# Performance work log

Measured on AMD Instinct MI355X. Metric: run time of the kernel, lower is better.

## Reference

```python
import jax, jax.numpy as jnp
import numpy as np

B, T, N, F_IN = 8, 288, 2000, 1
E, ID, H, K = 128, 16, 128, 20
FL = T // 2 + 1  # rfft length = in_len//2 + 1
EPS_NORM = 1e-12
EPS_LN = 1e-8


def setup_inputs() -> dict:
    key = jax.random.key(0)
    k0, k1, k2, k3, k4 = jax.random.split(key, 5)
    return {
        "x": jax.random.normal(k0, (B, T, N, F_IN), jnp.float32),
        "Ex": jax.random.normal(k1, (FL, E), jnp.float32),
        "nodes": jax.random.normal(k2, (N, ID), jnp.float32),
        "Wd": jax.random.normal(k3, (N, E + ID, H), jnp.float32),
        "Wxabs": jax.random.normal(k4, (H, H), jnp.float32),
    }


def reference(x, Ex, nodes, Wd, Wxabs):
    # [B,T,N,F] -> take feature 0 -> [B,N,T]
    xt = jnp.transpose(x[:, :, :, 0], (0, 2, 1))
    xf = jnp.abs(jnp.fft.rfft(xt, axis=-1))  # [B,N,FL]
    # F.normalize p=2 over dim=1 (nodes), then dim=2 (freq): x / max(||x||, eps)
    xf = xf / jnp.clip(jnp.sqrt(jnp.sum(xf * xf, axis=1, keepdims=True)), EPS_NORM)
    xf = xf / jnp.clip(jnp.sqrt(jnp.sum(xf * xf, axis=2, keepdims=True)), EPS_NORM)
    xe = jnp.matmul(xf, Ex)  # [B,N,E]
    # cat(): append static node identity embedding per batch element
    xk = jnp.concatenate(
        [xe, jnp.broadcast_to(nodes, (xe.shape[0], N, ID))], axis=-1
    )  # [B,N,E+ID]
    # per-node weight bmm: [N,B,E+ID] @ [N,E+ID,H] -> [B,N,H]
    x1 = jax.nn.relu(jnp.einsum('bnd,ndh->bnh', xk, Wd))
    # LayerNorm over last two dims [N,H], eps=1e-8, no affine
    mu = jnp.mean(x1, axis=(1, 2), keepdims=True)
    var = jnp.mean((x1 - mu) ** 2, axis=(1, 2), keepdims=True)
    x2 = (x1 - mu) / jnp.sqrt(var + EPS_LN)
    # dropout is identity at inference
    adp = jnp.einsum('bnh,hk->bnk', x2, Wxabs)  # convt
    adj = jnp.einsum('bnh,bmh->bnm', adp, x1)  # [B,N,N]
    adp = jax.nn.relu(adj)
    # dy_mask_graph: per-row topk over dim=2 (torch dim=1 of the [N,N] slice),
    # binary mask via scatter of ones, then elementwise mask
    _, idx = jax.lax.top_k(adp, K)  # [B,N,K]
    bi = jnp.arange(adp.shape[0])[:, None, None]
    ni = jnp.arange(N)[None, :, None]
    mask = jnp.zeros_like(adp).at[bi, ni, idx].set(1.0)
    adj_masked = adp * mask
    return jax.nn.softmax(adj_masked, axis=2)
```

## Files before the change

kernel.cpp:

```cpp
#include <hip/hip_runtime.h>
#include <math.h>

#define BB 8
#define TT 288
#define NN 2000
#define FLEN 145
#define EE 128
#define IDD 16
#define HH 128
#define DKK 144
#define KTOP 20

typedef _Float16 half8 __attribute__((ext_vector_type(8)));
typedef float f32x4 __attribute__((ext_vector_type(4)));
typedef unsigned short ushort_t;

#define OFF_TW  ((size_t)0)
#define SZ_TW   ((size_t)TT*FLEN*2)
#define OFF_XF  (OFF_TW + SZ_TW)
#define SZ_XF   ((size_t)BB*FLEN*NN)
#define OFF_ICN (OFF_XF + SZ_XF)
#define OFF_IRN (OFF_ICN + (size_t)BB*FLEN)
#define OFF_XE  (OFF_IRN + (size_t)BB*NN)
#define SZ_BNH  ((size_t)BB*NN*HH)
#define OFF_X1  (OFF_XE + SZ_BNH)
#define OFF_ADP (OFF_X1 + SZ_BNH)
#define OFF_CSW (OFF_ADP + SZ_BNH)
#define OFF_LNS (OFF_CSW + HH)
#define OFF_LNF (OFF_LNS + 16)


__device__ __forceinline__ float wredSum(float v) {
#pragma unroll
  for (int o = 32; o > 0; o >>= 1) v += __shfl_down(v, o, 64);
  return v;
}
__device__ __forceinline__ float wredMax(float v) {
#pragma unroll
  for (int o = 32; o > 0; o >>= 1) v = fmaxf(v, __shfl_down(v, o, 64));
  return v;
}
__device__ __forceinline__ float wredSumAll(float v) {
#pragma unroll
  for (int o = 32; o > 0; o >>= 1) v += __shfl_xor(v, o, 64);
  return v;
}
__device__ __forceinline__ float wredMaxAll(float v) {
#pragma unroll
  for (int o = 32; o > 0; o >>= 1) v = fmaxf(v, __shfl_xor(v, o, 64));
  return v;
}

__device__ __forceinline__ void split16(float v, ushort_t& hi, ushort_t& lo) {
  _Float16 h = (_Float16)v;
  _Float16 l = (_Float16)(v - (float)h);
  union { _Float16 f; ushort_t u; } a, b;
  a.f = h; b.f = l;
  hi = a.u; lo = b.u;
}

__global__ void k_init(const float* __restrict__ Wx, float* __restrict__ csw,
                       float* __restrict__ lns) {
  int k = threadIdx.x;
  float s = 0.f;
  for (int h = 0; h < HH; ++h) s += Wx[h * HH + k];
  csw[k] = s;
  if (k < 16) lns[k] = 0.f;
}

__global__ void k_tw(float* __restrict__ tw) {
  int id = blockIdx.x * 256 + threadIdx.x;
  if (id >= TT * FLEN) return;
  int t = id / FLEN, f = id % FLEN;
  int r = (t * f) % TT;
  double th = -2.0 * 3.14159265358979323846 * (double)r / (double)TT;
  tw[2 * id]     = (float)cos(th);
  tw[2 * id + 1] = (float)sin(th);
}

__global__ void k_dft(const float* __restrict__ x, const float* __restrict__ tw,
                      float* __restrict__ xf) {
  __shared__ __align__(16) float Xs[16][128];
  __shared__ __align__(16) float TWs[16][32][2];
  const int b = blockIdx.z;
  const int f0 = blockIdx.y * 32;
  const int n0 = blockIdx.x * 128;
  const int tid = threadIdx.x;
  const int tn = tid & 31;
  const int tf = tid >> 5;
  float ar[4][4] = {}, ai[4][4] = {};
  for (int t0 = 0; t0 < TT; t0 += 16) {
    __syncthreads();
    for (int l = tid; l < 512; l += 256) {
      int row = l >> 5, q = l & 31;
      int n = n0 + q * 4;
      const float* src = x + ((size_t)b * TT + (t0 + row)) * NN + n;
      float4 v = make_float4(0, 0, 0, 0);
      if (n + 3 < NN) v = *(const float4*)src;
      else {
        if (n + 0 < NN) v.x = src[0];
        if (n + 1 < NN) v.y = src[1];
        if (n + 2 < NN) v.z = src[2];
        if (n + 3 < NN) v.w = src[3];
      }
      *(float4*)&Xs[row][q * 4] = v;
    }
    for (int l = tid; l < 512; l += 256) {
      int row = l >> 5, ff = l & 31;
      int f = f0 + ff;
      float2 cs = make_float2(0, 0);
      if (f < FLEN) cs = *(const float2*)&tw[((size_t)(t0 + row) * FLEN + f) * 2];
      *(float2*)&TWs[row][ff][0] = cs;
    }
    __syncthreads();
#pragma unroll 4
    for (int t = 0; t < 16; ++t) {
      float4 xv = *(float4*)&Xs[t][tn * 4];
      float xx[4] = {xv.x, xv.y, xv.z, xv.w};
      float4 p0 = *(float4*)&TWs[t][tf * 4][0];
      float4 p1 = *(float4*)&TWs[t][tf * 4 + 2][0];
      float c[4] = {p0.x, p0.z, p1.x, p1.z};
      float s[4] = {p0.y, p0.w, p1.y, p1.w};
#pragma unroll
      for (int i = 0; i < 4; ++i)
#pragma unroll
        for (int j = 0; j < 4; ++j) {
          ar[i][j] = fmaf(xx[j], c[i], ar[i][j]);
          ai[i][j] = fmaf(xx[j], s[i], ai[i][j]);
        }
    }
  }
#pragma unroll
  for (int i = 0; i < 4; ++i) {
    int f = f0 + tf * 4 + i;
    if (f >= FLEN) continue;
    float* dst = &xf[((size_t)b * FLEN + f) * NN];
    float o[4];
#pragma unroll
    for (int j = 0; j < 4; ++j)
      o[j] = sqrtf(ar[i][j] * ar[i][j] + ai[i][j] * ai[i][j]);
    int n = n0 + tn * 4;
    if (n + 3 < NN) *(float4*)&dst[n] = make_float4(o[0], o[1], o[2], o[3]);
    else {
#pragma unroll
      for (int j = 0; j < 4; ++j) if (n + j < NN) dst[n + j] = o[j];
    }
  }
}

__global__ void k_colnorm(const float* __restrict__ xf, float* __restrict__ icn) {
  __shared__ float sc[4];
  int bf = blockIdx.x;
  const float* rowp = xf + (size_t)bf * NN;
  float s = 0.f;
  for (int i = threadIdx.x; i < NN; i += 256) { float v = rowp[i]; s = fmaf(v, v, s); }
  s = wredSum(s);
  int lane = threadIdx.x & 63, w = threadIdx.x >> 6;
  if (lane == 0) sc[w] = s;
  __syncthreads();
  if (threadIdx.x == 0)
    icn[bf] = 1.f / fmaxf(sqrtf(sc[0] + sc[1] + sc[2] + sc[3]), 1e-12f);
}

__global__ void k_rownorm(const float* __restrict__ xf, const float* __restrict__ icn,
                          float* __restrict__ irn) {
  int b = blockIdx.y;
  int n = blockIdx.x * 256 + threadIdx.x;
  if (n >= NN) return;
  float s = 0.f;
  for (int f = 0; f < FLEN; ++f) {
    float v = xf[((size_t)b * FLEN + f) * NN + n] * icn[b * FLEN + f];
    s = fmaf(v, v, s);
  }
  irn[b * NN + n] = 1.f / fmaxf(sqrtf(s), 1e-12f);
}

__global__ void k_xe(const float* __restrict__ xf, const float* __restrict__ icn,
                     const float* __restrict__ irn, const float* __restrict__ Ex,
                     float* __restrict__ xe) {
  __shared__ __align__(16) float As[16][64];
  __shared__ __align__(16) float Bs[16][128];
  const int b = blockIdx.y;
  const int n0 = blockIdx.x * 64;
  const int tid = threadIdx.x;
  const int tn = tid >> 4, te = tid & 15;
  float acc[4][8] = {};
  for (int f0 = 0; f0 < 160; f0 += 16) {
    __syncthreads();
    {
      int kt = tid >> 4, q = tid & 15;
      int f = f0 + kt;
      int n = n0 + q * 4;
      float4 v = make_float4(0, 0, 0, 0);
      if (f < FLEN) {
        float ic = icn[b * FLEN + f];
        const float* src = &xf[((size_t)b * FLEN + f) * NN + n];
        if (n + 3 < NN) v = *(const float4*)src;
        else {
          if (n + 0 < NN) v.x = src[0];
          if (n + 1 < NN) v.y = src[1];
          if (n + 2 < NN) v.z = src[2];
          if (n + 3 < NN) v.w = src[3];
        }
        v.x *= ic; v.y *= ic; v.z *= ic; v.w *= ic;
      }
      *(float4*)&As[kt][q * 4] = v;
    }
    for (int l = tid; l < 512; l += 256) {
      int kt = l >> 5, q = l & 31;
      int f = f0 + kt;
      float4 v = make_float4(0, 0, 0, 0);
      if (f < FLEN) v = *(const float4*)&Ex[(size_t)f * EE + q * 4];
      *(float4*)&Bs[kt][q * 4] = v;
    }
    __syncthreads();
#pragma unroll
    for (int k = 0; k < 16; ++k) {
      float4 a  = *(float4*)&As[k][tn * 4];
      float4 b0 = *(float4*)&Bs[k][te * 4];
      float4 b1 = *(float4*)&Bs[k][64 + te * 4];
      float av[4] = {a.x, a.y, a.z, a.w};
      float bv[8] = {b0.x, b0.y, b0.z, b0.w, b1.x, b1.y, b1.z, b1.w};
#pragma unroll
      for (int i = 0; i < 4; ++i)
#pragma unroll
        for (int j = 0; j < 8; ++j)
          acc[i][j] = fmaf(av[i], bv[j], acc[i][j]);
    }
  }
#pragma unroll
  for (int i = 0; i < 4; ++i) {
    int n = n0 + tn * 4 + i;
    if (n >= NN) continue;
    float sc = irn[b * NN + n];
    float* dst = &xe[((size_t)b * NN + n) * EE];
    *(float4*)&dst[te * 4] =
        make_float4(acc[i][0] * sc, acc[i][1] * sc, acc[i][2] * sc, acc[i][3] * sc);
    *(float4*)&dst[64 + te * 4] =
        make_float4(acc[i][4] * sc, acc[i][5] * sc, acc[i][6] * sc, acc[i][7] * sc);
  }
}

__global__ void k_x1(const float* xe, const float* __restrict__ nodes,
                     const float* __restrict__ Wd, float* __restrict__ x1,
                     ushort_t* x1hl) {
  __shared__ __align__(16) float xk[8][DKK];
  __shared__ float red[4][32][33];
  const int n = blockIdx.x;
  const int tid = threadIdx.x;
  {
    int b = tid >> 5, q = tid & 31;
    *(float4*)&xk[b][q * 4] = *(const float4*)&xe[((size_t)b * NN + n) * EE + q * 4];
  }
  if (tid < 128) {
    int b = tid >> 4, i = tid & 15;
    xk[b][EE + i] = nodes[(size_t)n * IDD + i];
  }
  __syncthreads();
  const int h4 = tid & 31;
  const int dg = tid >> 5;
  float acc[8][4] = {};
  for (int d = dg; d < DKK; d += 8) {
    float4 wv = *(const float4*)&Wd[((size_t)n * DKK + d) * HH + h4 * 4];
#pragma unroll
    for (int b = 0; b < 8; ++b) {
      float xv = xk[b][d];
      acc[b][0] = fmaf(xv, wv.x, acc[b][0]);
      acc[b][1] = fmaf(xv, wv.y, acc[b][1]);
      acc[b][2] = fmaf(xv, wv.z, acc[b][2]);
      acc[b][3] = fmaf(xv, wv.w, acc[b][3]);
    }
  }
#pragma unroll
  for (int b = 0; b < 8; ++b)
#pragma unroll
    for (int j = 0; j < 4; ++j)
      acc[b][j] += __shfl_xor(acc[b][j], 32, 64);
  const int wv_ = tid >> 6, lane = tid & 63;
  if (lane < 32) {
#pragma unroll
    for (int b = 0; b < 8; ++b)
#pragma unroll
      for (int j = 0; j < 4; ++j)
        red[wv_][lane][b * 4 + j] = acc[b][j];
  }
  __syncthreads();
  const size_t tbase = (size_t)(n >> 4) * 4096 + (size_t)(n & 15) * 8;
#pragma unroll
  for (int o = 0; o < 4; ++o) {
    int idx = tid + o * 256;
    int b = idx >> 7, h = idx & 127;
    float s = red[0][h >> 2][b * 4 + (h & 3)] + red[1][h >> 2][b * 4 + (h & 3)] +
              red[2][h >> 2][b * 4 + (h & 3)] + red[3][h >> 2][b * 4 + (h & 3)];
    s = fmaxf(s, 0.f);
    x1[((size_t)b * NN + n) * HH + h] = s;
    ushort_t hi, lo;
    split16(s, hi, lo);
    size_t slot = (size_t)b * (125 * 4096) + tbase +
                  (size_t)((h >> 5) * 512 + ((h >> 3) & 3) * 128 + (h & 7));
    x1hl[slot] = hi;
    x1hl[slot + 2048] = lo;
  }
}

__global__ void k_ln_stats(const float* __restrict__ x1, float* __restrict__ lns) {
  __shared__ float sc[4], sc2[4];
  int b = blockIdx.y, chunk = blockIdx.x;
  const float* base = x1 + (size_t)b * NN * HH + (size_t)chunk * 8000;
  float s = 0.f, s2 = 0.f;
  for (int i = threadIdx.x; i < 8000; i += 256) {
    float v = base[i];
    s += v; s2 = fmaf(v, v, s2);
  }
  s = wredSum(s); s2 = wredSum(s2);
  int lane = threadIdx.x & 63, w = threadIdx.x >> 6;
  if (lane == 0) { sc[w] = s; sc2[w] = s2; }
  __syncthreads();
  if (threadIdx.x == 0) {
    atomicAdd(&lns[b], sc[0] + sc[1] + sc[2] + sc[3]);
    atomicAdd(&lns[8 + b], sc2[0] + sc2[1] + sc2[2] + sc2[3]);
  }
}

__global__ void k_ln_final(const float* __restrict__ lns, float* __restrict__ lnf) {
  int b = threadIdx.x;
  if (b < 8) {
    float cnt = (float)(NN * HH);
    float mu = lns[b] / cnt;
    float var = fmaxf(lns[8 + b] / cnt - mu * mu, 0.f);
    lnf[b] = mu;
    lnf[8 + b] = 1.f / sqrtf(var + 1e-8f);
  }
}

__global__ void k_adp(const float* __restrict__ x1, const float* __restrict__ Wx,
                      const float* __restrict__ csw, const float* __restrict__ lnf,
                      ushort_t* __restrict__ adphl) {
  __shared__ __align__(16) float As[16][64];
  __shared__ __align__(16) float Bs[16][128];
  const int r0 = blockIdx.x * 64;
  const int tid = threadIdx.x;
  const int tn = tid >> 4, te = tid & 15;
  float acc[4][8] = {};
  for (int k0 = 0; k0 < HH; k0 += 16) {
    __syncthreads();
    {
      int rr = tid >> 2, kq = tid & 3;
      float4 v = *(const float4*)&x1[(size_t)(r0 + rr) * HH + k0 + kq * 4];
      As[kq * 4 + 0][rr] = v.x;
      As[kq * 4 + 1][rr] = v.y;
      As[kq * 4 + 2][rr] = v.z;
      As[kq * 4 + 3][rr] = v.w;
    }
    for (int l = tid; l < 512; l += 256) {
      int kt = l >> 5, q = l & 31;
      *(float4*)&Bs[kt][q * 4] = *(const float4*)&Wx[(size_t)(k0 + kt) * HH + q * 4];
    }
    __syncthreads();
#pragma unroll
    for (int k = 0; k < 16; ++k) {
      float4 a  = *(float4*)&As[k][tn * 4];
      float4 b0 = *(float4*)&Bs[k][te * 4];
      float4 b1 = *(float4*)&Bs[k][64 + te * 4];
      float av[4] = {a.x, a.y, a.z, a.w};
      float bv[8] = {b0.x, b0.y, b0.z, b0.w, b1.x, b1.y, b1.z, b1.w};
#pragma unroll
      for (int i = 0; i < 4; ++i)
#pragma unroll
        for (int j = 0; j < 8; ++j)
          acc[i][j] = fmaf(av[i], bv[j], acc[i][j]);
    }
  }
  float4 c0 = *(const float4*)&csw[te * 4];
  float4 c1 = *(const float4*)&csw[64 + te * 4];
  float cw[8] = {c0.x, c0.y, c0.z, c0.w, c1.x, c1.y, c1.z, c1.w};
  const int c0k = te * 4, c1k = 64 + te * 4;
  const size_t o0r = (size_t)((c0k >> 5) * 512 + ((c0k >> 3) & 3) * 128 + (c0k & 7));
  const size_t o1r = (size_t)((c1k >> 5) * 512 + ((c1k >> 3) & 3) * 128 + (c1k & 7));
#pragma unroll
  for (int i = 0; i < 4; ++i) {
    int r = r0 + tn * 4 + i;
    int b = r / NN, n = r % NN;
    float mu = lnf[b], isd = lnf[8 + b];
    ushort_t hi[8], lo[8];
#pragma unroll
    for (int j = 0; j < 8; ++j) {
      float o = (acc[i][j] - mu * cw[j]) * isd;
      split16(o, hi[j], lo[j]);
    }
    size_t slot = (size_t)b * (125 * 4096) + (size_t)(n >> 4) * 4096 +
                  (size_t)(n & 15) * 8;
    ushort4 u;
    u.x = hi[0]; u.y = hi[1]; u.z = hi[2]; u.w = hi[3];
    *(ushort4*)&adphl[slot + o0r] = u;
    u.x = hi[4]; u.y = hi[5]; u.z = hi[6]; u.w = hi[7];
    *(ushort4*)&adphl[slot + o1r] = u;
    u.x = lo[0]; u.y = lo[1]; u.z = lo[2]; u.w = lo[3];
    *(ushort4*)&adphl[slot + 2048 + o0r] = u;
    u.x = lo[4]; u.y = lo[5]; u.z = lo[6]; u.w = lo[7];
    *(ushort4*)&adphl[slot + 2048 + o1r] = u;
  }
}

__global__ __launch_bounds__(256, 2) void k_adjT(
    const ushort_t* __restrict__ adphl, const ushort_t* __restrict__ x1hl,
    float* __restrict__ out) {
  const int b = blockIdx.z;
  const int tA = blockIdx.y;
  const int n0 = tA * 16;
  const int tid = threadIdx.x;
  const int w = tid >> 6;
  const int lane = tid & 63;
  const int quad = lane >> 4, r16 = lane & 15;
  const int lq = quad * 128 + r16 * 8;

  half8 Ah[4], Al[4];
  {
    const ushort_t* abase = adphl + ((size_t)(b * 125 + tA)) * 4096 + lq;
#pragma unroll
    for (int ks = 0; ks < 4; ++ks) {
      Ah[ks] = *(const half8*)(abase + ks * 512);
      Al[ks] = *(const half8*)(abase + 2048 + ks * 512);
    }
  }
  const int mbase = blockIdx.x * 512 + w * 128;
  const ushort_t* Bb = x1hl + (size_t)b * (125 * 4096) + lq;
  float* obase = out + ((size_t)(b * NN + n0 + quad * 4)) * NN;

  half8 Bh0[4], Bl0[4], Bh1[4], Bl1[4];

#define LOADB(I, BH, BL)                                                      \
  {                                                                           \
    int tB_ = (mbase + (I) * 16) >> 4;                                        \
    if (tB_ > 124) tB_ = 124;         \
    const ushort_t* bb_ = Bb + (size_t)tB_ * 4096;                            \
    BH[0] = *(const half8*)(bb_);        BL[0] = *(const half8*)(bb_ + 2048); \
    BH[1] = *(const half8*)(bb_ + 512);  BL[1] = *(const half8*)(bb_ + 2560); \
    BH[2] = *(const half8*)(bb_ + 1024); BL[2] = *(const half8*)(bb_ + 3072); \
    BH[3] = *(const half8*)(bb_ + 1536); BL[3] = *(const half8*)(bb_ + 3584); \
  }

#define STEP(I, BH, BL, BH2, BL2)                                             \
  {                                                                           \
    if ((I) < 7) LOADB((I) + 1, BH2, BL2);                                    \
    __builtin_amdgcn_sched_barrier(0);      \
    f32x4 acc = (f32x4){0.f, 0.f, 0.f, 0.f};                                  \
    _Pragma("unroll")                                                         \
    for (int ks = 0; ks < 4; ++ks) {                                          \
      acc = __builtin_amdgcn_mfma_f32_16x16x32_f16(Ah[ks], BH[ks], acc, 0, 0, 0); \
      acc = __builtin_amdgcn_mfma_f32_16x16x32_f16(Ah[ks], BL[ks], acc, 0, 0, 0); \
      acc = __builtin_amdgcn_mfma_f32_16x16x32_f16(Al[ks], BH[ks], acc, 0, 0, 0); \
    }                                                                         \
    int mt_ = mbase + (I) * 16 + r16;                                         \
    if (mt_ < NN) {                                                           \
      _Pragma("unroll")                                                       \
      for (int reg = 0; reg < 4; ++reg)                                       \
        obase[(size_t)reg * NN + mt_] = fmaxf(acc[reg], 0.f);                 \
    }                                                                         \
  }

  LOADB(0, Bh0, Bl0);
  STEP(0, Bh0, Bl0, Bh1, Bl1);
  STEP(1, Bh1, Bl1, Bh0, Bl0);
  STEP(2, Bh0, Bl0, Bh1, Bl1);
  STEP(3, Bh1, Bl1, Bh0, Bl0);
  STEP(4, Bh0, Bl0, Bh1, Bl1);
  STEP(5, Bh1, Bl1, Bh0, Bl0);
  STEP(6, Bh0, Bl0, Bh1, Bl1);
  STEP(7, Bh1, Bl1, Bh0, Bl0);
#undef STEP
#undef LOADB
}

__global__ __launch_bounds__(256, 4) void k_topsm(float* out) {
  __shared__ float scrV[4][64];
  __shared__ int scrI[4][64];
  const int tid = threadIdx.x;
  const int w = tid >> 6, lane = tid & 63;
  const int r = blockIdx.x * 4 + w;
  float* g = out + (size_t)r * NN;

  f32x4 V[8];
#pragma unroll
  for (int j = 0; j < 8; ++j) {
    int m0 = j * 256 + lane * 4;
    if (m0 < NN) V[j] = *(const f32x4*)&g[m0];
    else V[j] = (f32x4){-1.f, -1.f, -1.f, -1.f};
  }

  float mx = -1.f, cp = 0.f;
#pragma unroll
  for (int j = 0; j < 8; ++j)
#pragma unroll
    for (int e = 0; e < 4; ++e) {
      mx = fmaxf(mx, V[j][e]);
      cp += (V[j][e] > 0.f) ? 1.f : 0.f;
    }
  const float m = wredMaxAll(mx);
  const float cpos = wredSumAll(cp);
  const float em = expf(-m);

  if (cpos <= 20.5f) {
    float s = 0.f;
#pragma unroll
    for (int j = 0; j < 8; ++j)
#pragma unroll
      for (int e = 0; e < 4; ++e)
        if (V[j][e] > 0.f) s += expf(V[j][e] - m);
    s = wredSumAll(s);
    const float invD = 1.f / (s + (2000.f - cpos) * em);
    const float defv = em * invD;
#pragma unroll
    for (int j = 0; j < 8; ++j) {
      int m0 = j * 256 + lane * 4;
      if (m0 >= NN) continue;
      float4 o;
      o.x = (V[j][0] > 0.f) ? expf(V[j][0] - m) * invD : defv;
      o.y = (V[j][1] > 0.f) ? expf(V[j][1] - m) * invD : defv;
      o.z = (V[j][2] > 0.f) ? expf(V[j][2] - m) * invD : defv;
      o.w = (V[j][3] > 0.f) ? expf(V[j][3] - m) * invD : defv;
      *(float4*)&g[m0] = o;
    }
  } else {
    float tval = 0.f, cf = cpos;
    if (cpos > 64.5f) {
      float tlo = 0.f, thi = m;
      bool found = false;
      for (int it = 0; it < 64 && !found; ++it) {
        float mid = (it < 12)
            ? 0.5f * (tlo + thi)
            : __uint_as_float((__float_as_uint(tlo) + __float_as_uint(thi)) >> 1);
        float c = 0.f;
#pragma unroll
        for (int j = 0; j < 8; ++j)
#pragma unroll
          for (int e = 0; e < 4; ++e)
            c += (V[j][e] > mid) ? 1.f : 0.f;
        c = wredSumAll(c);
        if (c > 64.5f) tlo = mid;
        else if (c < 19.5f) thi = mid;
        else { tval = mid; cf = c; found = true; }
      }
      if (!found) { tval = tlo; cf = 64.f; }
    }
    int cI = (int)(cf + 0.5f);
    if (cI > 64) cI = 64;

    float* sv = scrV[w];
    int* si = scrI[w];
    int base = 0;
#pragma unroll
    for (int j = 0; j < 8; ++j)
#pragma unroll
      for (int e = 0; e < 4; ++e) {
        bool p = V[j][e] > tval;
        unsigned long long msk = __ballot(p);
        if (p) {
          int pos = base + (int)__popcll(msk & ((1ull << lane) - 1ull));
          if (pos < 64) { sv[pos] = V[j][e]; si[pos] = j * 256 + lane * 4 + e; }
        }
        base += (int)__popcll(msk);
      }
    asm volatile("s_waitcnt lgkmcnt(0)" ::: "memory");

    float cv = (lane < cI) ? sv[lane] : -1.f;
    int ci = (lane < cI) ? si[lane] : 0x7fffffff;
#pragma unroll
    for (int k = 2; k <= 64; k <<= 1)
#pragma unroll
      for (int j = k >> 1; j > 0; j >>= 1) {
        float ov = __shfl_xor(cv, j, 64);
        int oi = __shfl_xor(ci, j, 64);
        bool otherBetter = (ov > cv) || (ov == cv && oi < ci);
        bool iAmLow = (lane & j) == 0;
        bool desc = (lane & k) == 0;
        bool take = (desc == iAmLow) ? otherBetter : !otherBetter;
        if (take) { cv = ov; ci = oi; }
      }
    const float t20 = __shfl(cv, 19, 64);
    float e20 = (lane < 20) ? expf(cv - m) : 0.f;
    const float s20 = wredSumAll(e20);
    const float invD = 1.f / (s20 + (2000.f - 20.f) * em);
    const float defv = em * invD;
#pragma unroll
    for (int j = 0; j < 8; ++j) {
      int m0 = j * 256 + lane * 4;
      if (m0 >= NN) continue;
      float4 o;
      o.x = (V[j][0] >= t20) ? expf(V[j][0] - m) * invD : defv;
      o.y = (V[j][1] >= t20) ? expf(V[j][1] - m) * invD : defv;
      o.z = (V[j][2] >= t20) ? expf(V[j][2] - m) * invD : defv;
      o.w = (V[j][3] >= t20) ? expf(V[j][3] - m) * invD : defv;
      *(float4*)&g[m0] = o;
    }
  }
}

extern "C" void kernel_launch(void* const* d_in, const int* in_sizes, int n_in,
                              void* d_out, int out_size, void* d_ws, size_t ws_size,
                              hipStream_t stream) {
  const float* x     = (const float*)d_in[0];
  const float* Ex    = (const float*)d_in[1];
  const float* nodes = (const float*)d_in[2];
  const float* Wd    = (const float*)d_in[3];
  const float* Wx    = (const float*)d_in[4];
  float* out = (float*)d_out;
  float* w = (float*)d_ws;
  float* tw  = w + OFF_TW;
  float* xf  = w + OFF_XF;
  float* icn = w + OFF_ICN;
  float* irn = w + OFF_IRN;
  float* xe  = w + OFF_XE;
  float* x1  = w + OFF_X1;
  float* csw = w + OFF_CSW;
  float* lns = w + OFF_LNS;
  float* lnf = w + OFF_LNF;
  ushort_t* adphl = (ushort_t*)(w + OFF_ADP);
  ushort_t* x1hl  = (ushort_t*)(w + OFF_XE);

  k_init<<<1, 128, 0, stream>>>(Wx, csw, lns);
  k_tw<<<(TT * FLEN + 255) / 256, 256, 0, stream>>>(tw);
  k_dft<<<dim3(16, 5, BB), 256, 0, stream>>>(x, tw, xf);
  k_colnorm<<<BB * FLEN, 256, 0, stream>>>(xf, icn);
  k_rownorm<<<dim3(8, BB), 256, 0, stream>>>(xf, icn, irn);
  k_xe<<<dim3(32, BB), 256, 0, stream>>>(xf, icn, irn, Ex, xe);
  k_x1<<<NN, 256, 0, stream>>>(xe, nodes, Wd, x1, x1hl);
  k_ln_stats<<<dim3(32, BB), 256, 0, stream>>>(x1, lns);
  k_ln_final<<<1, 64, 0, stream>>>(lns, lnf);
  k_adp<<<250, 256, 0, stream>>>(x1, Wx, csw, lnf, adphl);
  k_adjT<<<dim3(4, 125, BB), 256, 0, stream>>>(adphl, x1hl, out);
  k_topsm<<<(BB * NN) / 4, 256, 0, stream>>>(out);
}
```

Before: 490.7 us.

## Fuse adjacency GEMM with top-k softmax and merge tiny init kernels

The adjacency MFMA kernel now computes a full 16-row by 2000-column strip per 512-thread block and keeps it in registers. It then does the per-row max, count, bisection threshold search, candidate collection and softmax in place, so the intermediate [B,N,N] matrix is no longer written and re-read by a separate top-k pass. The small init and LN-finalize kernels are folded into the twiddle and adp kernels to cut launches. In exchange, register pressure goes up, the grid has only 1000 blocks, and the bisection loop needs block-wide syncs.

```diff
diff --git a/kernel.cpp b/kernel.cpp
--- a/kernel.cpp
+++ b/kernel.cpp
@@ -35,19 +35,9 @@
   for (int o = 32; o > 0; o >>= 1) v += __shfl_down(v, o, 64);
   return v;
 }
-__device__ __forceinline__ float wredMax(float v) {
-#pragma unroll
-  for (int o = 32; o > 0; o >>= 1) v = fmaxf(v, __shfl_down(v, o, 64));
-  return v;
-}
 __device__ __forceinline__ float wredSumAll(float v) {
 #pragma unroll
   for (int o = 32; o > 0; o >>= 1) v += __shfl_xor(v, o, 64);
-  return v;
-}
-__device__ __forceinline__ float wredMaxAll(float v) {
-#pragma unroll
-  for (int o = 32; o > 0; o >>= 1) v = fmaxf(v, __shfl_xor(v, o, 64));
   return v;
 }
 
@@ -59,16 +49,15 @@
   hi = a.u; lo = b.u;
 }
 
-__global__ void k_init(const float* __restrict__ Wx, float* __restrict__ csw,
-                       float* __restrict__ lns) {
-  int k = threadIdx.x;
-  float s = 0.f;
-  for (int h = 0; h < HH; ++h) s += Wx[h * HH + k];
-  csw[k] = s;
-  if (k < 16) lns[k] = 0.f;
-}
-
-__global__ void k_tw(float* __restrict__ tw) {
+__global__ void k_tw(const float* __restrict__ Wx, float* __restrict__ tw,
+                     float* __restrict__ csw, float* __restrict__ lns) {
+  if (blockIdx.x == 0 && threadIdx.x < 128) {
+    int k = threadIdx.x;
+    float s = 0.f;
+    for (int h = 0; h < HH; ++h) s += Wx[h * HH + k];
+    csw[k] = s;
+    if (k < 16) lns[k] = 0.f;
+  }
   int id = blockIdx.x * 256 + threadIdx.x;
   if (id >= TT * FLEN) return;
   int t = id / FLEN, f = id % FLEN;
@@ -322,19 +311,8 @@
   }
 }
 
-__global__ void k_ln_final(const float* __restrict__ lns, float* __restrict__ lnf) {
-  int b = threadIdx.x;
-  if (b < 8) {
-    float cnt = (float)(NN * HH);
-    float mu = lns[b] / cnt;
-    float var = fmaxf(lns[8 + b] / cnt - mu * mu, 0.f);
-    lnf[b] = mu;
-    lnf[8 + b] = 1.f / sqrtf(var + 1e-8f);
-  }
-}
-
 __global__ void k_adp(const float* __restrict__ x1, const float* __restrict__ Wx,
-                      const float* __restrict__ csw, const float* __restrict__ lnf,
+                      const float* __restrict__ csw, const float* __restrict__ lns,
                       ushort_t* __restrict__ adphl) {
   __shared__ __align__(16) float As[16][64];
   __shared__ __align__(16) float Bs[16][128];
@@ -381,7 +359,10 @@
   for (int i = 0; i < 4; ++i) {
     int r = r0 + tn * 4 + i;
     int b = r / NN, n = r % NN;
-    float mu = lnf[b], isd = lnf[8 + b];
+    float cnt = (float)(NN * HH);
+    float mu = lns[b] / cnt;
+    float var = fmaxf(lns[8 + b] / cnt - mu * mu, 0.f);
+    float isd = 1.f / sqrtf(var + 1e-8f);
     ushort_t hi[8], lo[8];
 #pragma unroll
     for (int j = 0; j < 8; ++j) {
@@ -402,11 +383,18 @@
   }
 }
 
-__global__ __launch_bounds__(256, 2) void k_adjT(
+__global__ __launch_bounds__(512, 2) void k_adjsm(
     const ushort_t* __restrict__ adphl, const ushort_t* __restrict__ x1hl,
     float* __restrict__ out) {
-  const int b = blockIdx.z;
-  const int tA = blockIdx.y;
+  __shared__ float wmax[8][16], wcnt0[8][16], wcntB[8][16], wexp[8][16];
+  __shared__ int doneP[16];
+  __shared__ int candCnt[16];
+  __shared__ float candV[16][64];
+  __shared__ int candI[16][64];
+  __shared__ float pthr[16], pm[16], pinv[16], pdef[16];
+
+  const int b = blockIdx.y;
+  const int tA = blockIdx.x;
   const int n0 = tA * 16;
   const int tid = threadIdx.x;
   const int w = tid >> 6;
@@ -423,17 +411,15 @@
       Al[ks] = *(const half8*)(abase + 2048 + ks * 512);
     }
   }
-  const int mbase = blockIdx.x * 512 + w * 128;
   const ushort_t* Bb = x1hl + (size_t)b * (125 * 4096) + lq;
-  float* obase = out + ((size_t)(b * NN + n0 + quad * 4)) * NN;
-
+  f32x4 V[16];
   half8 Bh0[4], Bl0[4], Bh1[4], Bl1[4];
 
 #define LOADB(I, BH, BL)                                                      \
   {                                                                           \
-    int tB_ = (mbase + (I) * 16) >> 4;                                        \
-    if (tB_ > 124) tB_ = 124;         \
-    const ushort_t* bb_ = Bb + (size_t)tB_ * 4096;                            \
+    int tl_ = w + 8 * (I);                                                    \
+    if (tl_ > 124) tl_ = 124;                                                 \
+    const ushort_t* bb_ = Bb + (size_t)tl_ * 4096;                            \
     BH[0] = *(const half8*)(bb_);        BL[0] = *(const half8*)(bb_ + 2048); \
     BH[1] = *(const half8*)(bb_ + 512);  BL[1] = *(const half8*)(bb_ + 2560); \
     BH[2] = *(const half8*)(bb_ + 1024); BL[2] = *(const half8*)(bb_ + 3072); \
@@ -442,8 +428,8 @@
 
 #define STEP(I, BH, BL, BH2, BL2)                                             \
   {                                                                           \
-    if ((I) < 7) LOADB((I) + 1, BH2, BL2);                                    \
-    __builtin_amdgcn_sched_barrier(0);      \
+    if ((I) < 15) LOADB((I) + 1, BH2, BL2);                                   \
+    __builtin_amdgcn_sched_barrier(0);                                        \
     f32x4 acc = (f32x4){0.f, 0.f, 0.f, 0.f};                                  \
     _Pragma("unroll")                                                         \
     for (int ks = 0; ks < 4; ++ks) {                                          \
@@ -451,147 +437,225 @@
       acc = __builtin_amdgcn_mfma_f32_16x16x32_f16(Ah[ks], BL[ks], acc, 0, 0, 0); \
       acc = __builtin_amdgcn_mfma_f32_16x16x32_f16(Al[ks], BH[ks], acc, 0, 0, 0); \
     }                                                                         \
-    int mt_ = mbase + (I) * 16 + r16;                                         \
-    if (mt_ < NN) {                                                           \
-      _Pragma("unroll")                                                       \
-      for (int reg = 0; reg < 4; ++reg)                                       \
-        obase[(size_t)reg * NN + mt_] = fmaxf(acc[reg], 0.f);                 \
-    }                                                                         \
+    bool vld_ = (w + 8 * (I)) <= 124;                                         \
+    _Pragma("unroll")                                                         \
+    for (int reg = 0; reg < 4; ++reg)                                         \
+      V[(I)][reg] = vld_ ? fmaxf(acc[reg], 0.f) : -1.f;                       \
   }
 
   LOADB(0, Bh0, Bl0);
-  STEP(0, Bh0, Bl0, Bh1, Bl1);
-  STEP(1, Bh1, Bl1, Bh0, Bl0);
-  STEP(2, Bh0, Bl0, Bh1, Bl1);
-  STEP(3, Bh1, Bl1, Bh0, Bl0);
-  STEP(4, Bh0, Bl0, Bh1, Bl1);
-  STEP(5, Bh1, Bl1, Bh0, Bl0);
-  STEP(6, Bh0, Bl0, Bh1, Bl1);
-  STEP(7, Bh1, Bl1, Bh0, Bl0);
+  STEP(0,  Bh0, Bl0, Bh1, Bl1);
+  STEP(1,  Bh1, Bl1, Bh0, Bl0);
+  STEP(2,  Bh0, Bl0, Bh1, Bl1);
+  STEP(3,  Bh1, Bl1, Bh0, Bl0);
+  STEP(4,  Bh0, Bl0, Bh1, Bl1);
+  STEP(5,  Bh1, Bl1, Bh0, Bl0);
+  STEP(6,  Bh0, Bl0, Bh1, Bl1);
+  STEP(7,  Bh1, Bl1, Bh0, Bl0);
+  STEP(8,  Bh0, Bl0, Bh1, Bl1);
+  STEP(9,  Bh1, Bl1, Bh0, Bl0);
+  STEP(10, Bh0, Bl0, Bh1, Bl1);
+  STEP(11, Bh1, Bl1, Bh0, Bl0);
+  STEP(12, Bh0, Bl0, Bh1, Bl1);
+  STEP(13, Bh1, Bl1, Bh0, Bl0);
+  STEP(14, Bh0, Bl0, Bh1, Bl1);
+  STEP(15, Bh1, Bl1, Bh0, Bl0);
 #undef STEP
 #undef LOADB
-}
-
-__global__ __launch_bounds__(256, 4) void k_topsm(float* out) {
-  __shared__ float scrV[4][64];
-  __shared__ int scrI[4][64];
-  const int tid = threadIdx.x;
-  const int w = tid >> 6, lane = tid & 63;
-  const int r = blockIdx.x * 4 + w;
-  float* g = out + (size_t)r * NN;
-
-  f32x4 V[8];
-#pragma unroll
-  for (int j = 0; j < 8; ++j) {
-    int m0 = j * 256 + lane * 4;
-    if (m0 < NN) V[j] = *(const f32x4*)&g[m0];
-    else V[j] = (f32x4){-1.f, -1.f, -1.f, -1.f};
-  }
-
-  float mx = -1.f, cp = 0.f;
-#pragma unroll
-  for (int j = 0; j < 8; ++j)
-#pragma unroll
-    for (int e = 0; e < 4; ++e) {
-      mx = fmaxf(mx, V[j][e]);
-      cp += (V[j][e] > 0.f) ? 1.f : 0.f;
-    }
-  const float m = wredMaxAll(mx);
-  const float cpos = wredSumAll(cp);
-  const float em = expf(-m);
-
-  if (cpos <= 20.5f) {
-    float s = 0.f;
-#pragma unroll
-    for (int j = 0; j < 8; ++j)
-#pragma unroll
-      for (int e = 0; e < 4; ++e)
-        if (V[j][e] > 0.f) s += expf(V[j][e] - m);
-    s = wredSumAll(s);
-    const float invD = 1.f / (s + (2000.f - cpos) * em);
-    const float defv = em * invD;
-#pragma unroll
-    for (int j = 0; j < 8; ++j) {
-      int m0 = j * 256 + lane * 4;
-      if (m0 >= NN) continue;
-      float4 o;
-      o.x = (V[j][0] > 0.f) ? expf(V[j][0] - m) * invD : defv;
-      o.y = (V[j][1] > 0.f) ? expf(V[j][1] - m) * invD : defv;
-      o.z = (V[j][2] > 0.f) ? expf(V[j][2] - m) * invD : defv;
-      o.w = (V[j][3] > 0.f) ? expf(V[j][3] - m) * invD : defv;
-      *(float4*)&g[m0] = o;
-    }
-  } else {
-    float tval = 0.f, cf = cpos;
-    if (cpos > 64.5f) {
-      float tlo = 0.f, thi = m;
-      bool found = false;
-      for (int it = 0; it < 64 && !found; ++it) {
-        float mid = (it < 12)
-            ? 0.5f * (tlo + thi)
-            : __uint_as_float((__float_as_uint(tlo) + __float_as_uint(thi)) >> 1);
-        float c = 0.f;
-#pragma unroll
-        for (int j = 0; j < 8; ++j)
-#pragma unroll
-          for (int e = 0; e < 4; ++e)
-            c += (V[j][e] > mid) ? 1.f : 0.f;
-        c = wredSumAll(c);
-        if (c > 64.5f) tlo = mid;
-        else if (c < 19.5f) thi = mid;
-        else { tval = mid; cf = c; found = true; }
+
+  float mx4[4] = {-1.f, -1.f, -1.f, -1.f}, cp4[4] = {0.f, 0.f, 0.f, 0.f};
+#pragma unroll
+  for (int i = 0; i < 16; ++i)
+#pragma unroll
+    for (int reg = 0; reg < 4; ++reg) {
+      mx4[reg] = fmaxf(mx4[reg], V[i][reg]);
+      cp4[reg] += (V[i][reg] > 0.f) ? 1.f : 0.f;
+    }
+#pragma unroll
+  for (int o = 8; o > 0; o >>= 1)
+#pragma unroll
+    for (int reg = 0; reg < 4; ++reg) {
+      mx4[reg] = fmaxf(mx4[reg], __shfl_xor(mx4[reg], o, 64));
+      cp4[reg] += __shfl_xor(cp4[reg], o, 64);
+    }
+  if (r16 == 0) {
+#pragma unroll
+    for (int reg = 0; reg < 4; ++reg) {
+      wmax[w][quad * 4 + reg] = mx4[reg];
+      wcnt0[w][quad * 4 + reg] = cp4[reg];
+    }
+  }
+  __syncthreads();
+  float m4[4], c4[4];
+#pragma unroll
+  for (int reg = 0; reg < 4; ++reg) {
+    int row = quad * 4 + reg;
+    float m = wmax[0][row], c = wcnt0[0][row];
+    for (int ww = 1; ww < 8; ++ww) { m = fmaxf(m, wmax[ww][row]); c += wcnt0[ww][row]; }
+    m4[reg] = m; c4[reg] = c;
+  }
+
+  float se4[4] = {0.f, 0.f, 0.f, 0.f};
+#pragma unroll
+  for (int reg = 0; reg < 4; ++reg) {
+    if (c4[reg] <= 20.5f) {
+#pragma unroll
+      for (int i = 0; i < 16; ++i) {
+        float v = V[i][reg];
+        if (v > 0.f) se4[reg] += expf(v - m4[reg]);
       }
-      if (!found) { tval = tlo; cf = 64.f; }
-    }
-    int cI = (int)(cf + 0.5f);
-    if (cI > 64) cI = 64;
-
-    float* sv = scrV[w];
-    int* si = scrI[w];
-    int base = 0;
-#pragma unroll
-    for (int j = 0; j < 8; ++j)
-#pragma unroll
-      for (int e = 0; e < 4; ++e) {
-        bool p = V[j][e] > tval;
-        unsigned long long msk = __ballot(p);
-        if (p) {
-          int pos = base + (int)__popcll(msk & ((1ull << lane) - 1ull));
-          if (pos < 64) { sv[pos] = V[j][e]; si[pos] = j * 256 + lane * 4 + e; }
+    }
+  }
+#pragma unroll
+  for (int o = 8; o > 0; o >>= 1)
+#pragma unroll
+    for (int reg = 0; reg < 4; ++reg) se4[reg] += __shfl_xor(se4[reg], o, 64);
+  if (r16 == 0)
+#pragma unroll
+    for (int reg = 0; reg < 4; ++reg) wexp[w][quad * 4 + reg] = se4[reg];
+
+  float tlo4[4], thi4[4], tval4[4];
+  int done4[4];
+#pragma unroll
+  for (int reg = 0; reg < 4; ++reg) {
+    tval4[reg] = 0.f;
+    tlo4[reg] = 0.f; thi4[reg] = m4[reg];
+    done4[reg] = (c4[reg] <= 64.5f) ? 1 : 0;
+  }
+  if (w == 0 && r16 == 0)
+#pragma unroll
+    for (int reg = 0; reg < 4; ++reg) doneP[quad * 4 + reg] = done4[reg];
+  __syncthreads();
+  {
+    bool ad = true;
+    for (int rr = 0; rr < 16; ++rr) if (!doneP[rr]) ad = false;
+    if (!ad) {
+      for (int it = 0; it < 64; ++it) {
+        float mid4[4];
+#pragma unroll
+        for (int reg = 0; reg < 4; ++reg)
+          mid4[reg] = (it < 12)
+              ? 0.5f * (tlo4[reg] + thi4[reg])
+              : __uint_as_float((__float_as_uint(tlo4[reg]) + __float_as_uint(thi4[reg])) >> 1);
+        float cc4[4] = {0.f, 0.f, 0.f, 0.f};
+#pragma unroll
+        for (int i = 0; i < 16; ++i)
+#pragma unroll
+          for (int reg = 0; reg < 4; ++reg)
+            cc4[reg] += (V[i][reg] > mid4[reg]) ? 1.f : 0.f;
+#pragma unroll
+        for (int o = 8; o > 0; o >>= 1)
+#pragma unroll
+          for (int reg = 0; reg < 4; ++reg) cc4[reg] += __shfl_xor(cc4[reg], o, 64);
+        if (r16 == 0)
+#pragma unroll
+          for (int reg = 0; reg < 4; ++reg) wcntB[w][quad * 4 + reg] = cc4[reg];
+        __syncthreads();
+#pragma unroll
+        for (int reg = 0; reg < 4; ++reg) {
+          if (!done4[reg]) {
+            int row = quad * 4 + reg;
+            float c = 0.f;
+            for (int ww = 0; ww < 8; ++ww) c += wcntB[ww][row];
+            if (c > 64.5f) tlo4[reg] = mid4[reg];
+            else if (c < 19.5f) thi4[reg] = mid4[reg];
+            else { tval4[reg] = mid4[reg]; done4[reg] = 1; }
+            if (it == 63 && !done4[reg]) { tval4[reg] = tlo4[reg]; done4[reg] = 1; }
+          }
         }
-        base += (int)__popcll(msk);
+        if (w == 0 && r16 == 0)
+#pragma unroll
+          for (int reg = 0; reg < 4; ++reg) doneP[quad * 4 + reg] = done4[reg];
+        __syncthreads();
+        bool ad2 = true;
+        for (int rr = 0; rr < 16; ++rr) if (!doneP[rr]) ad2 = false;
+        if (ad2) break;
       }
-    asm volatile("s_waitcnt lgkmcnt(0)" ::: "memory");
-
-    float cv = (lane < cI) ? sv[lane] : -1.f;
-    int ci = (lane < cI) ? si[lane] : 0x7fffffff;
-#pragma unroll
-    for (int k = 2; k <= 64; k <<= 1)
-#pragma unroll
-      for (int j = k >> 1; j > 0; j >>= 1) {
-        float ov = __shfl_xor(cv, j, 64);
-        int oi = __shfl_xor(ci, j, 64);
-        bool otherBetter = (ov > cv) || (ov == cv && oi < ci);
-        bool iAmLow = (lane & j) == 0;
-        bool desc = (lane & k) == 0;
-        bool take = (desc == iAmLow) ? otherBetter : !otherBetter;
-        if (take) { cv = ov; ci = oi; }
+    }
+  }
+
+  if (tid < 16) candCnt[tid] = 0;
+  __syncthreads();
+#pragma unroll
+  for (int reg = 0; reg < 4; ++reg) {
+    if (c4[reg] > 20.5f) {
+      int row = quad * 4 + reg;
+#pragma unroll
+      for (int i = 0; i < 16; ++i) {
+        float v = V[i][reg];
+        if (v > tval4[reg]) {
+          int idx = atomicAdd(&candCnt[row], 1);
+          if (idx < 64) {
+            candV[row][idx] = v;
+            candI[row][idx] = (w + 8 * i) * 16 + r16;
+          }
+        }
       }
-    const float t20 = __shfl(cv, 19, 64);
-    float e20 = (lane < 20) ? expf(cv - m) : 0.f;
-    const float s20 = wredSumAll(e20);
-    const float invD = 1.f / (s20 + (2000.f - 20.f) * em);
-    const float defv = em * invD;
-#pragma unroll
-    for (int j = 0; j < 8; ++j) {
-      int m0 = j * 256 + lane * 4;
-      if (m0 >= NN) continue;
-      float4 o;
-      o.x = (V[j][0] >= t20) ? expf(V[j][0] - m) * invD : defv;
-      o.y = (V[j][1] >= t20) ? expf(V[j][1] - m) * invD : defv;
-      o.z = (V[j][2] >= t20) ? expf(V[j][2] - m) * invD : defv;
-      o.w = (V[j][3] >= t20) ? expf(V[j][3] - m) * invD : defv;
-      *(float4*)&g[m0] = o;
+    }
+  }
+  __syncthreads();
+
+  for (int rr = 0; rr < 2; ++rr) {
+    int row = w * 2 + rr;
+    float m = wmax[0][row];
+    for (int ww = 1; ww < 8; ++ww) m = fmaxf(m, wmax[ww][row]);
+    float cpos = 0.f;
+    for (int ww = 0; ww < 8; ++ww) cpos += wcnt0[ww][row];
+    float em = expf(-m);
+    if (cpos <= 20.5f) {
+      float s = 0.f;
+      for (int ww = 0; ww < 8; ++ww) s += wexp[ww][row];
+      float invD = 1.f / (s + (2000.f - cpos) * em);
+      if (lane == 0) {
+        pthr[row] = __uint_as_float(1u);
+        pm[row] = m; pinv[row] = invD; pdef[row] = em * invD;
+      }
+    } else {
+      int cI = candCnt[row]; if (cI > 64) cI = 64;
+      float cv = (lane < cI) ? candV[row][lane] : -1.f;
+      int ci = (lane < cI) ? candI[row][lane] : 0x7fffffff;
+#pragma unroll
+      for (int k = 2; k <= 64; k <<= 1)
+#pragma unroll
+        for (int j = k >> 1; j > 0; j >>= 1) {
+          float ov = __shfl_xor(cv, j, 64);
+          int oi = __shfl_xor(ci, j, 64);
+          bool otherBetter = (ov > cv) || (ov == cv && oi < ci);
+          bool iAmLow = (lane & j) == 0;
+          bool desc = (lane & k) == 0;
+          bool take = (desc == iAmLow) ? otherBetter : !otherBetter;
+          if (take) { cv = ov; ci = oi; }
+        }
+      float t20 = __shfl(cv, 19, 64);
+      float e20 = (lane < 20) ? expf(cv - m) : 0.f;
+      float s20 = wredSumAll(e20);
+      float invD = 1.f / (s20 + (2000.f - 20.f) * em);
+      if (lane == 0) {
+        pthr[row] = t20; pm[row] = m; pinv[row] = invD; pdef[row] = em * invD;
+      }
+    }
+  }
+  __syncthreads();
+
+  float thr4[4], pmm4[4], piv4[4], pdv4[4];
+#pragma unroll
+  for (int reg = 0; reg < 4; ++reg) {
+    int row = quad * 4 + reg;
+    thr4[reg] = pthr[row]; pmm4[reg] = pm[row];
+    piv4[reg] = pinv[row]; pdv4[reg] = pdef[row];
+  }
+  const size_t ob0 = ((size_t)(b * NN + n0)) * NN;
+#pragma unroll
+  for (int i = 0; i < 16; ++i) {
+    int tl = w + 8 * i;
+    if (tl > 124) continue;
+    int mcol = tl * 16 + r16;
+#pragma unroll
+    for (int reg = 0; reg < 4; ++reg) {
+      int row = quad * 4 + reg;
+      float v = V[i][reg];
+      float o = (v >= thr4[reg]) ? expf(v - pmm4[reg]) * piv4[reg] : pdv4[reg];
+      out[ob0 + (size_t)row * NN + mcol] = o;
     }
   }
 }
@@ -614,20 +678,16 @@
   float* x1  = w + OFF_X1;
   float* csw = w + OFF_CSW;
   float* lns = w + OFF_LNS;
-  float* lnf = w + OFF_LNF;
   ushort_t* adphl = (ushort_t*)(w + OFF_ADP);
   ushort_t* x1hl  = (ushort_t*)(w + OFF_XE);
 
-  k_init<<<1, 128, 0, stream>>>(Wx, csw, lns);
-  k_tw<<<(TT * FLEN + 255) / 256, 256, 0, stream>>>(tw);
+  k_tw<<<(TT * FLEN + 255) / 256, 256, 0, stream>>>(Wx, tw, csw, lns);
   k_dft<<<dim3(16, 5, BB), 256, 0, stream>>>(x, tw, xf);
   k_colnorm<<<BB * FLEN, 256, 0, stream>>>(xf, icn);
   k_rownorm<<<dim3(8, BB), 256, 0, stream>>>(xf, icn, irn);
   k_xe<<<dim3(32, BB), 256, 0, stream>>>(xf, icn, irn, Ex, xe);
   k_x1<<<NN, 256, 0, stream>>>(xe, nodes, Wd, x1, x1hl);
   k_ln_stats<<<dim3(32, BB), 256, 0, stream>>>(x1, lns);
-  k_ln_final<<<1, 64, 0, stream>>>(lns, lnf);
-  k_adp<<<250, 256, 0, stream>>>(x1, Wx, csw, lnf, adphl);
-  k_adjT<<<dim3(4, 125, BB), 256, 0, stream>>>(adphl, x1hl, out);
-  k_topsm<<<(BB * NN) / 4, 256, 0, stream>>>(out);
-}
+  k_adp<<<250, 256, 0, stream>>>(x1, Wx, csw, lns, adphl);
+  k_adjsm<<<dim3(125, BB), 512, 0, stream>>>(adphl, x1hl, out);
+}
```

Result: slower. 535.3 us (+9.1%).
